# Optimization experiments

Measured on AMD Instinct MI355X. Metric: run time of the kernel, lower is better.

## Reference

```python
import jax, jax.numpy as jnp
import numpy as np

DIM = 512
HEADS = 8
HD = DIM // HEADS          # head_dim = 64
GROUPS = 32                # GroupNorm groups
EPS = 1e-5
SCALE = HD ** -0.25        # double-scale: applied to both q and k
B, H, W, L, CTX = 8, 32, 32, 77, 768


def setup_inputs() -> dict:
    key = jax.random.key(0)
    ks = jax.random.split(key, 6)
    return {
        "x": jax.random.normal(ks[0], (B, DIM, H, W), jnp.float32),
        "context": jax.random.normal(ks[1], (B, L, CTX), jnp.float32),
        "gn_gamma": jnp.ones((DIM,), jnp.float32),
        "gn_beta": jnp.zeros((DIM,), jnp.float32),
        "qkv_w": jax.random.normal(ks[2], (3 * DIM, DIM), jnp.float32) * 0.02,
        "qkv_b": jnp.zeros((3 * DIM,), jnp.float32),
        "ckv_w": jax.random.normal(ks[3], (2 * DIM, CTX), jnp.float32) * 0.02,
        "ckv_b": jnp.zeros((2 * DIM,), jnp.float32),
        "proj_w": jax.random.normal(ks[4], (DIM, DIM), jnp.float32) * 0.02,
        "proj_b": jnp.zeros((DIM,), jnp.float32),
    }


def _group_norm(x, gamma, beta):
    b, c, h, w = x.shape
    xr = x.reshape(b, GROUPS, c // GROUPS, h, w)
    mu = xr.mean(axis=(2, 3, 4), keepdims=True)
    var = xr.var(axis=(2, 3, 4), keepdims=True)
    xr = (xr - mu) * jax.lax.rsqrt(var + EPS)
    return xr.reshape(b, c, h, w) * gamma[None, :, None, None] + beta[None, :, None, None]


def reference(x, context, gn_gamma, gn_beta, qkv_w, qkv_b, ckv_w, ckv_b, proj_w, proj_b):
    b, c, h, w = x.shape
    n, d = HEADS, HD
    identity = x

    xn = _group_norm(x, gn_gamma, gn_beta)
    # 1x1 conv == channel GEMM. qkv: [b, 3*dim, h*w] -> [b, 3, n, d, hw]
    qkv = jnp.einsum('bchw,oc->bohw', xn, qkv_w) + qkv_b[None, :, None, None]
    qkv = qkv.reshape(b, 3, n, d, h * w)
    q, k, v = qkv[:, 0], qkv[:, 1], qkv[:, 2]   # each [b, n, d, hw]

    # context kv: Linear(context_dim, 2*dim) -> [b, L, 2, n, d] -> [b, n, d, L]
    ckv = jnp.einsum('blc,oc->blo', context, ckv_w) + ckv_b
    ckv = ckv.reshape(b, -1, 2, n, d)
    ck = jnp.transpose(ckv[:, :, 0], (0, 2, 3, 1))  # [b, n, d, L]
    cv = jnp.transpose(ckv[:, :, 1], (0, 2, 3, 1))
    k = jnp.concatenate([ck, k], axis=-1)           # [b, n, d, L+hw]
    v = jnp.concatenate([cv, v], axis=-1)

    # attn = (q^T * s) @ (k * s); softmax over keys
    attn = jnp.einsum('bndq,bndk->bnqk', q * SCALE, k * SCALE)
    attn = jax.nn.softmax(attn, axis=-1)
    out = jnp.einsum('bndk,bnqk->bndq', v, attn).reshape(b, c, h, w)

    out = jnp.einsum('bchw,oc->bohw', out, proj_w) + proj_b[None, :, None, None]
    return out + identity
```

## Files before the change

kernel.cpp:

```cpp
#include <hip/hip_runtime.h>

#define B_ 8
#define DIM_ 512
#define HEADS_ 8
#define HD_ 64
#define HW_ 1024
#define L_ 77
#define LP_ 80
#define CTX_ 768
#define KV_ 1101
#define KVP_ 1152
#define NPAD_ 51
#define CTX0_ 1024
#define SC_QK 0.42466089f

typedef __attribute__((ext_vector_type(8))) short bf16x8;
typedef __attribute__((ext_vector_type(4))) float f32x4;
typedef __attribute__((ext_vector_type(4))) unsigned short u16x4;

__device__ __forceinline__ unsigned short f2bf(float f) {
  union { float f; unsigned int u; } c; c.f = f;
  unsigned int u = c.u;
  return (unsigned short)((u + 0x7fffu + ((u >> 16) & 1u)) >> 16);
}
__device__ __forceinline__ float bf2f(unsigned short h) {
  union { unsigned int u; float f; } c; c.u = ((unsigned int)h) << 16;
  return c.f;
}

#define GLD_LDS16(gsrc, ldst) \
  __builtin_amdgcn_global_load_lds((const __attribute__((address_space(1))) void*)(gsrc), \
                                   (__attribute__((address_space(3))) void*)(ldst), 16, 0, 0)

__global__ __launch_bounds__(256) void prep_k(const float* __restrict__ qkv_w,
                                              const float* __restrict__ ckv_w,
                                              const float* __restrict__ proj_w,
                                              const float* __restrict__ ctx,
                                              unsigned short* __restrict__ dq,
                                              unsigned short* __restrict__ dc,
                                              unsigned short* __restrict__ dp,
                                              unsigned short* __restrict__ ctx_bf,
                                              unsigned short* __restrict__ k_s,
                                              unsigned short* __restrict__ vT) {
  int bid = blockIdx.x;
  int tid = threadIdx.x;
  if (bid < 1792) {
    int i = bid * 256 + tid;
    const float* src;
    unsigned short* dst;
    int off;
    if (i < 196608) { src = qkv_w; dst = dq; off = i; }
    else if (i < 393216) { src = ckv_w; dst = dc; off = i - 196608; }
    else { src = proj_w; dst = dp; off = i - 393216; }
    float4 v = *(const float4*)(src + (size_t)off * 4);
    u16x4 o;
    o[0] = f2bf(v.x); o[1] = f2bf(v.y); o[2] = f2bf(v.z); o[3] = f2bf(v.w);
    *(u16x4*)(dst + (size_t)off * 4) = o;
  } else if (bid < 2272) {
    int i = (bid - 1792) * 256 + tid;
    int idx = i * 4;
    int b = idx / (LP_ * CTX_);
    int rem = idx - b * (LP_ * CTX_);
    int l = rem / CTX_;
    int c = rem - l * CTX_;
    float4 v = make_float4(0.f, 0.f, 0.f, 0.f);
    if (l < L_) v = *(const float4*)&ctx[((size_t)b * L_ + l) * CTX_ + c];
    u16x4 o;
    o[0] = f2bf(v.x); o[1] = f2bf(v.y); o[2] = f2bf(v.z); o[3] = f2bf(v.w);
    *(u16x4*)(ctx_bf + idx) = o;
  } else {
    int i = (bid - 2272) * 256 + tid;
    int bh = i / (NPAD_ * 64);
    int rem = i - bh * (NPAD_ * 64);
    int row = KV_ + rem / 64;
    int d = rem & 63;
    k_s[((size_t)bh * KVP_ + row) * HD_ + d] = 0;
    vT[((size_t)bh * HD_ + d) * KVP_ + row] = 0;
  }
}

__global__ __launch_bounds__(256) void gnorm_k(const float* __restrict__ x,
                                               const float* __restrict__ gamma,
                                               const float* __restrict__ beta,
                                               unsigned short* __restrict__ xn_t) {
  __shared__ unsigned short xs[16][1032];
  __shared__ float red[8];
  const int tid = threadIdx.x;
  const int b = blockIdx.x >> 5, g = blockIdx.x & 31;
  const float* xp = x + ((size_t)b * DIM_ + g * 16) * HW_;
  float sum = 0.f, ssq = 0.f;
#pragma unroll
  for (int i = 0; i < 16; ++i) {
    float4 v = *(const float4*)&xp[i * HW_ + tid * 4];
    sum += v.x + v.y + v.z + v.w;
    ssq += v.x * v.x + v.y * v.y + v.z * v.z + v.w * v.w;
    xs[i][tid * 4 + 0] = f2bf(v.x);
    xs[i][tid * 4 + 1] = f2bf(v.y);
    xs[i][tid * 4 + 2] = f2bf(v.z);
    xs[i][tid * 4 + 3] = f2bf(v.w);
  }
#pragma unroll
  for (int off = 32; off >= 1; off >>= 1) {
    sum += __shfl_xor(sum, off, 64);
    ssq += __shfl_xor(ssq, off, 64);
  }
  if ((tid & 63) == 0) { red[(tid >> 6) * 2] = sum; red[(tid >> 6) * 2 + 1] = ssq; }
  __syncthreads();
  sum = red[0] + red[2] + red[4] + red[6];
  ssq = red[1] + red[3] + red[5] + red[7];
  float mu = sum * (1.f / 16384.f);
  float rstd = rsqrtf(ssq * (1.f / 16384.f) - mu * mu + 1e-5f);
  float a[16], c[16];
#pragma unroll
  for (int ci = 0; ci < 16; ++ci) {
    float gm = gamma[g * 16 + ci], bt = beta[g * 16 + ci];
    a[ci] = rstd * gm;
    c[ci] = bt - mu * rstd * gm;
  }
#pragma unroll
  for (int t = 0; t < 4; ++t) {
    int hw = tid + t * 256;
    unsigned short tmp[16];
#pragma unroll
    for (int ci = 0; ci < 16; ++ci)
      tmp[ci] = f2bf(bf2f(xs[ci][hw]) * a[ci] + c[ci]);
    unsigned int w[8];
#pragma unroll
    for (int j = 0; j < 8; ++j) w[j] = (unsigned int)tmp[2 * j] | ((unsigned int)tmp[2 * j + 1] << 16);
    unsigned short* dptr = &xn_t[((size_t)b * HW_ + hw) * DIM_ + g * 16];
    *(uint4*)dptr = make_uint4(w[0], w[1], w[2], w[3]);
    *(uint4*)(dptr + 8) = make_uint4(w[4], w[5], w[6], w[7]);
  }
}

template <int MODE, int BM, int BN>
__device__ __forceinline__ void gemm_body(int bid,
                                          const unsigned short* __restrict__ A,
                                          const unsigned short* __restrict__ Bt,
                                          int M, int N, int K,
                                          const float* __restrict__ bias,
                                          unsigned short* __restrict__ out_q,
                                          unsigned short* __restrict__ out_k,
                                          unsigned short* __restrict__ out_v,
                                          const float* __restrict__ xres,
                                          float* __restrict__ outf,
                                          unsigned short* sm) {
  constexpr int MR = BM / 32;
  constexpr int NR = BN / 32;
  constexpr int SLOADS = BM / 32 + BN / 32;
  unsigned short* As0 = sm;
  unsigned short* Bs0 = sm + 2 * BM * 64;
  const int tid = threadIdx.x;
  const int wid = tid >> 6, lane = tid & 63;
  const int lr = lane & 15, lg = lane >> 4;
  const int ntn = N / BN;
  const int tm = bid / ntn, tn = bid - tm * ntn;
  const int m0 = tm * BM, n0 = tn * BN;
  const int wr = wid >> 1, wc = wid & 1;
  f32x4 acc[MR][NR] = {};
  const int nkt = K >> 6;

  auto stage = [&](int bi, int kk) {
#pragma unroll
    for (int i = 0; i < BM / 32; ++i) {
      int c = i * 256 + tid;
      int row = c >> 3, ch = (c & 7) ^ (row & 7);
      GLD_LDS16(A + (size_t)(m0 + row) * K + kk + ch * 8,
                As0 + (size_t)bi * BM * 64 + (size_t)(i * 256 + wid * 64) * 8);
    }
#pragma unroll
    for (int i = 0; i < BN / 32; ++i) {
      int c = i * 256 + tid;
      int row = c >> 3, ch = (c & 7) ^ (row & 7);
      GLD_LDS16(Bt + (size_t)(n0 + row) * K + kk + ch * 8,
                Bs0 + (size_t)bi * BN * 64 + (size_t)(i * 256 + wid * 64) * 8);
    }
  };

  __builtin_amdgcn_sched_barrier(0);
  stage(0, 0);
  __builtin_amdgcn_sched_barrier(0);
  if (nkt > 1) stage(1, 64);
  __builtin_amdgcn_sched_barrier(0);

  for (int kt = 0; kt < nkt; ++kt) {
    if (kt < nkt - 1) {
      if constexpr (SLOADS == 8)      asm volatile("s_waitcnt vmcnt(8)" ::: "memory");
      else if constexpr (SLOADS == 6) asm volatile("s_waitcnt vmcnt(6)" ::: "memory");
      else                            asm volatile("s_waitcnt vmcnt(0)" ::: "memory");
    } else {
      asm volatile("s_waitcnt vmcnt(0)" ::: "memory");
    }
    __builtin_amdgcn_sched_barrier(0);
    __builtin_amdgcn_s_barrier();
    __builtin_amdgcn_sched_barrier(0);
    const unsigned short* Ab = As0 + (kt & 1) * BM * 64;
    const unsigned short* Bb = Bs0 + (kt & 1) * BN * 64;
#pragma unroll
    for (int ks = 0; ks < 2; ++ks) {
      bf16x8 af[MR], bf[NR];
#pragma unroll
      for (int mi = 0; mi < MR; ++mi)
        af[mi] = *(const bf16x8*)&Ab[(wr * (BM / 2) + mi * 16 + lr) * 64 +
                                     (((ks * 4 + lg) ^ (lr & 7)) * 8)];
#pragma unroll
      for (int nj = 0; nj < NR; ++nj)
        bf[nj] = *(const bf16x8*)&Bb[(wc * (BN / 2) + nj * 16 + lr) * 64 +
                                     (((ks * 4 + lg) ^ (lr & 7)) * 8)];
#pragma unroll
      for (int mi = 0; mi < MR; ++mi)
#pragma unroll
        for (int nj = 0; nj < NR; ++nj)
          acc[mi][nj] = __builtin_amdgcn_mfma_f32_16x16x32_bf16(af[mi], bf[nj], acc[mi][nj], 0, 0, 0);
    }
    asm volatile("s_waitcnt lgkmcnt(0)" ::: "memory");
    __builtin_amdgcn_sched_barrier(0);
    __builtin_amdgcn_s_barrier();
    __builtin_amdgcn_sched_barrier(0);
    if (kt + 2 < nkt) stage(kt & 1, (kt + 2) << 6);
  }

  if constexpr (MODE == 0) {
    const int which = n0 >> 9;
    const int bb = m0 >> 10;
    const int qibase = m0 & 1023;
    if (which == 2) {
      uint2* Vt = (uint2*)sm;
#pragma unroll
      for (int mi = 0; mi < MR; ++mi) {
#pragma unroll
        for (int nj = 0; nj < NR; ++nj) {
          int col = wc * 64 + nj * 16 + lr;
          float b = bias[n0 + col];
          unsigned int w0, w1;
          float v0 = acc[mi][nj][0] + b, v1 = acc[mi][nj][1] + b;
          float v2 = acc[mi][nj][2] + b, v3 = acc[mi][nj][3] + b;
          asm("v_cvt_pk_bf16_f32 %0, %1, %2" : "=v"(w0) : "v"(v0), "v"(v1));
          asm("v_cvt_pk_bf16_f32 %0, %1, %2" : "=v"(w1) : "v"(v2), "v"(v3));
          int chunk = (wr * 16 + mi * 4 + lg) ^ (lr * 2);
          Vt[col * 32 + chunk] = make_uint2(w0, w1);
        }
      }
      __syncthreads();
#pragma unroll
      for (int it = 0; it < 8; ++it) {
        int col = wid * 32 + it * 4 + lg;
        uint4 val = *(uint4*)&Vt[col * 32 + ((lr * 2) ^ ((col & 15) * 2))];
        int colg = n0 + col;
        int head = (colg >> 6) & 7, d = colg & 63;
        *(uint4*)&out_v[(((size_t)bb * HEADS_ + head) * HD_ + d) * KVP_ + qibase + lr * 8] = val;
      }
    } else {
      unsigned short* Tq = sm;
#pragma unroll
      for (int mi = 0; mi < MR; ++mi) {
#pragma unroll
        for (int nj = 0; nj < NR; ++nj) {
          int col = wc * 64 + nj * 16 + lr;
          float b = bias[n0 + col];
          int qr = wr * 64 + mi * 16 + lg * 4;
#pragma unroll
          for (int r = 0; r < 4; ++r)
            Tq[(qr + r) * 132 + col] = f2bf((acc[mi][nj][r] + b) * SC_QK);
        }
      }
      __syncthreads();
#pragma unroll
      for (int it = 0; it < 8; ++it) {
        int qi = wid * 32 + it * 4 + lg;
        uint2 lo = *(uint2*)&Tq[qi * 132 + lr * 8];
        uint2 hi = *(uint2*)&Tq[qi * 132 + lr * 8 + 4];
        uint4 val = make_uint4(lo.x, lo.y, hi.x, hi.y);
        int colg = n0 + lr * 8;
        int head = (colg >> 6) & 7, d = colg & 63;
        size_t bh = (size_t)bb * HEADS_ + head;
        if (which == 0)
          *(uint4*)&out_q[(bh * HW_ + qibase + qi) * HD_ + d] = val;
        else
          *(uint4*)&out_k[(bh * KVP_ + qibase + qi) * HD_ + d] = val;
      }
    }
  } else {
#pragma unroll
    for (int mi = 0; mi < MR; ++mi) {
#pragma unroll
      for (int nj = 0; nj < NR; ++nj) {
#pragma unroll
        for (int r = 0; r < 4; ++r) {
          int row = m0 + wr * (BM / 2) + mi * 16 + lg * 4 + r;
          int col = n0 + wc * (BN / 2) + nj * 16 + lr;
          float v = acc[mi][nj][r];
          if (MODE == 1) {
            int bb = row / LP_, l = row - bb * LP_;
            if (l < L_) {
              v += bias[col];
              int which = col >> 9, head = (col >> 6) & 7, d = col & 63;
              size_t bh = (size_t)bb * HEADS_ + head;
              if (which == 0) out_k[(bh * KVP_ + CTX0_ + l) * HD_ + d] = f2bf(v * SC_QK);
              else            out_v[(bh * HD_ + d) * KVP_ + CTX0_ + l] = f2bf(v);
            }
          } else {
            size_t idx = (size_t)(col >> 10) * (DIM_ * HW_) + (size_t)row * HW_ + (col & 1023);
            outf[idx] = v + bias[row] + xres[idx];
          }
        }
      }
    }
  }
}

__global__ __launch_bounds__(256, 2) void gemm_qkv_ckv_k(
    const unsigned short* __restrict__ xn_t, const unsigned short* __restrict__ qkvw,
    const unsigned short* __restrict__ ctx_bf, const unsigned short* __restrict__ ckvw,
    const float* __restrict__ qkv_b, const float* __restrict__ ckv_b,
    unsigned short* __restrict__ q_s, unsigned short* __restrict__ k_s,
    unsigned short* __restrict__ vT) {
  __shared__ unsigned short sm[2 * 256 * 64];
  int bid = blockIdx.x;
  if (bid < 80) {
    gemm_body<1, 64, 128>(bid, ctx_bf, ckvw, 640, 1024, 768, ckv_b,
                          nullptr, k_s, vT, nullptr, nullptr, sm);
  } else {
    int b = bid - 80;
    int b2 = (b & 7) * 96 + (b >> 3);
    gemm_body<0, 128, 128>(b2, xn_t, qkvw, 8192, 1536, 512, qkv_b,
                           q_s, k_s, vT, nullptr, nullptr, sm);
  }
}

__global__ __launch_bounds__(256, 2) void gemm_proj_k(
    const unsigned short* __restrict__ projw, const unsigned short* __restrict__ at_s,
    const float* __restrict__ proj_b, const float* __restrict__ x,
    float* __restrict__ out) {
  __shared__ unsigned short sm[2 * 192 * 64];
  gemm_body<2, 64, 128>(blockIdx.x, projw, at_s, 512, 8192, 512, proj_b,
                        nullptr, nullptr, nullptr, x, out, sm);
}

#define PSTRIDE 72

__device__ __forceinline__ void attn_tile64(const unsigned short* __restrict__ Ksb,
                                            const unsigned short* __restrict__ Vsb,
                                            const bf16x8 (&qf)[2][2], const bf16x8 ones,
                                            unsigned short* __restrict__ Pw0,
                                            unsigned short* __restrict__ Pw1,
                                            int lr, int lg,
                                            const int (&ro)[4], const int (&koff)[2],
                                            f32x4 (&lacc)[2], f32x4 (&acc)[2][4]) {
  f32x4 st[2][4] = {};
  __builtin_amdgcn_s_setprio(1);
#pragma unroll
  for (int ks = 0; ks < 2; ++ks) {
    bf16x8 kf[4];
#pragma unroll
    for (int t = 0; t < 4; ++t)
      kf[t] = *(const bf16x8*)&Ksb[ro[t] + koff[ks]];
#pragma unroll
    for (int t = 0; t < 4; ++t) {
      st[0][t] = __builtin_amdgcn_mfma_f32_16x16x32_bf16(kf[t], qf[0][ks], st[0][t], 0, 0, 0);
      st[1][t] = __builtin_amdgcn_mfma_f32_16x16x32_bf16(kf[t], qf[1][ks], st[1][t], 0, 0, 0);
    }
  }
  __builtin_amdgcn_s_setprio(0);
#pragma unroll
  for (int c = 0; c < 2; ++c) {
#pragma unroll
    for (int t = 0; t < 4; ++t)
#pragma unroll
      for (int r = 0; r < 4; ++r) st[c][t][r] = __builtin_amdgcn_exp2f(st[c][t][r]);
    unsigned short* Pw = c ? Pw1 : Pw0;
#pragma unroll
    for (int t = 0; t < 4; ++t) {
      unsigned int w0, w1;
      asm("v_cvt_pk_bf16_f32 %0, %1, %2" : "=v"(w0) : "v"(st[c][t][0]), "v"(st[c][t][1]));
      asm("v_cvt_pk_bf16_f32 %0, %1, %2" : "=v"(w1) : "v"(st[c][t][2]), "v"(st[c][t][3]));
      *(uint2*)&Pw[lr * PSTRIDE + t * 16 + lg * 4] = make_uint2(w0, w1);
    }
  }
#pragma unroll
  for (int ks = 0; ks < 2; ++ks) {
    bf16x8 pb0 = *(const bf16x8*)&Pw0[lr * PSTRIDE + ks * 32 + lg * 8];
    bf16x8 pb1 = *(const bf16x8*)&Pw1[lr * PSTRIDE + ks * 32 + lg * 8];
    __builtin_amdgcn_s_setprio(1);
    lacc[0] = __builtin_amdgcn_mfma_f32_16x16x32_bf16(ones, pb0, lacc[0], 0, 0, 0);
    lacc[1] = __builtin_amdgcn_mfma_f32_16x16x32_bf16(ones, pb1, lacc[1], 0, 0, 0);
#pragma unroll
    for (int dt = 0; dt < 4; ++dt) {
      bf16x8 vf = *(const bf16x8*)&Vsb[ro[dt] + koff[ks]];
      acc[0][dt] = __builtin_amdgcn_mfma_f32_16x16x32_bf16(vf, pb0, acc[0][dt], 0, 0, 0);
      acc[1][dt] = __builtin_amdgcn_mfma_f32_16x16x32_bf16(vf, pb1, acc[1][dt], 0, 0, 0);
    }
    __builtin_amdgcn_s_setprio(0);
  }
}

__global__ __launch_bounds__(256, 3) void attn_k(const unsigned short* __restrict__ q_s,
                                                 const unsigned short* __restrict__ k_s,
                                                 const unsigned short* __restrict__ vT,
                                                 unsigned short* __restrict__ at_s) {
  __shared__ unsigned short Ks[2][4096];
  __shared__ unsigned short Vs[2][4096];
  __shared__ unsigned short Pb[4][2][16 * PSTRIDE];
  const int tid = threadIdx.x;
  const int wid = tid >> 6, lane = tid & 63;
  const int lr = lane & 15, lg = lane >> 4;
  const int bidx = blockIdx.x;
  const int xcd = bidx & 7, idx = bidx >> 3;
  const int bh = xcd + 8 * (idx >> 3);
  const int qt = idx & 7;
  const int q0 = qt * 128 + wid * 32;
  const unsigned short* qp = q_s + (size_t)bh * HW_ * HD_;
  const unsigned short* kp = k_s + (size_t)bh * KVP_ * HD_;
  const unsigned short* vp = vT + (size_t)bh * HD_ * KVP_;
  unsigned short* Pw0 = Pb[wid][0];
  unsigned short* Pw1 = Pb[wid][1];

  const int srow = lane >> 3;
  const int schunk = (lane & 7) ^ srow;

  auto stage = [&](int bufi, int kk) {
#pragma unroll
    for (int jj = 0; jj < 2; ++jj) {
      GLD_LDS16(kp + (size_t)(kk + wid * 16 + jj * 8 + srow) * HD_ + schunk * 8,
                &Ks[bufi][(wid * 2 + jj) * 512]);
      GLD_LDS16(vp + (size_t)(wid * 16 + jj * 8 + srow) * KVP_ + kk + schunk * 8,
                &Vs[bufi][(wid * 2 + jj) * 512]);
    }
  };

  int ro[4], koff[2];
#pragma unroll
  for (int t = 0; t < 4; ++t) ro[t] = (t * 16 + lr) * 64;
#pragma unroll
  for (int ks = 0; ks < 2; ++ks) koff[ks] = ((ks * 4 + lg) ^ (lr & 7)) * 8;

  bf16x8 qf[2][2];
#pragma unroll
  for (int c = 0; c < 2; ++c)
#pragma unroll
    for (int ks = 0; ks < 2; ++ks)
      qf[c][ks] = *(const bf16x8*)&qp[(size_t)(q0 + c * 16 + lr) * HD_ + ks * 32 + lg * 8];

  bf16x8 ones;
#pragma unroll
  for (int j = 0; j < 8; ++j) ones[j] = (short)0x3F80;

  f32x4 acc[2][4] = {};
  f32x4 lacc[2] = {};

  __builtin_amdgcn_sched_barrier(0);
  stage(0, 0);
  __builtin_amdgcn_sched_barrier(0);
  stage(1, 64);
  __builtin_amdgcn_sched_barrier(0);

  int cur = 0;
  for (int it = 0; it < 17; ++it) {
    asm volatile("s_waitcnt vmcnt(4)" ::: "memory");
    __builtin_amdgcn_sched_barrier(0);
    __builtin_amdgcn_s_barrier();
    __builtin_amdgcn_sched_barrier(0);
    attn_tile64(Ks[cur], Vs[cur], qf, ones, Pw0, Pw1, lr, lg, ro, koff, lacc, acc);
    asm volatile("s_waitcnt lgkmcnt(0)" ::: "memory");
    __builtin_amdgcn_sched_barrier(0);
    __builtin_amdgcn_s_barrier();
    __builtin_amdgcn_sched_barrier(0);
    if (it < 16) stage(cur, (it + 2) * 64);
    cur ^= 1;
  }
  asm volatile("s_waitcnt vmcnt(0)" ::: "memory");
  __builtin_amdgcn_sched_barrier(0);
  __builtin_amdgcn_s_barrier();
  __builtin_amdgcn_sched_barrier(0);
  attn_tile64(Ks[cur], Vs[cur], qf, ones, Pw0, Pw1, lr, lg, ro, koff, lacc, acc);

  const int bb = bh >> 3, head = bh & 7;
#pragma unroll
  for (int c = 0; c < 2; ++c) {
    const float inv = 1.f / (lacc[c][0] - (float)NPAD_);
    const int qi = q0 + c * 16 + lr;
#pragma unroll
    for (int dt = 0; dt < 4; ++dt) {
      u16x4 o;
#pragma unroll
      for (int r = 0; r < 4; ++r) o[r] = f2bf(acc[c][dt][r] * inv);
      *(u16x4*)&at_s[((size_t)bb * HW_ + qi) * DIM_ + head * HD_ + dt * 16 + lg * 4] = o;
    }
  }
}

extern "C" void kernel_launch(void* const* d_in, const int* in_sizes, int n_in,
                              void* d_out, int out_size, void* d_ws, size_t ws_size,
                              hipStream_t stream) {
  (void)in_sizes; (void)n_in; (void)out_size; (void)ws_size;
  const float* x      = (const float*)d_in[0];
  const float* ctx    = (const float*)d_in[1];
  const float* gng    = (const float*)d_in[2];
  const float* gnb    = (const float*)d_in[3];
  const float* qkv_w  = (const float*)d_in[4];
  const float* qkv_b  = (const float*)d_in[5];
  const float* ckv_w  = (const float*)d_in[6];
  const float* ckv_b  = (const float*)d_in[7];
  const float* proj_w = (const float*)d_in[8];
  const float* proj_b = (const float*)d_in[9];
  float* out = (float*)d_out;

  char* ws = (char*)d_ws;
  size_t off = 0;
  auto alloc = [&](size_t bytes) {
    char* p = ws + off;
    off = (off + bytes + 255) & ~(size_t)255;
    return p;
  };
  unsigned short* xn_t    = (unsigned short*)alloc((size_t)B_ * HW_ * DIM_ * 2);
  unsigned short* ctx_bf  = (unsigned short*)alloc((size_t)B_ * LP_ * CTX_ * 2);
  unsigned short* qkvw_bf = (unsigned short*)alloc((size_t)3 * DIM_ * DIM_ * 2);
  unsigned short* ckvw_bf = (unsigned short*)alloc((size_t)2 * DIM_ * CTX_ * 2);
  unsigned short* projw_bf= (unsigned short*)alloc((size_t)DIM_ * DIM_ * 2);
  unsigned short* q_s     = (unsigned short*)alloc((size_t)64 * HW_ * HD_ * 2);
  unsigned short* k_s     = (unsigned short*)alloc((size_t)64 * KVP_ * HD_ * 2);
  unsigned short* vT      = (unsigned short*)alloc((size_t)64 * HD_ * KVP_ * 2);
  unsigned short* at_s    = (unsigned short*)alloc((size_t)B_ * HW_ * DIM_ * 2);

  prep_k<<<3088, 256, 0, stream>>>(qkv_w, ckv_w, proj_w, ctx,
                                   qkvw_bf, ckvw_bf, projw_bf, ctx_bf, k_s, vT);
  gnorm_k<<<256, 256, 0, stream>>>(x, gng, gnb, xn_t);
  gemm_qkv_ckv_k<<<848, 256, 0, stream>>>(xn_t, qkvw_bf, ctx_bf, ckvw_bf,
                                          qkv_b, ckv_b, q_s, k_s, vT);
  attn_k<<<512, 256, 0, stream>>>(q_s, k_s, vT, at_s);
  gemm_proj_k<<<512, 256, 0, stream>>>(projw_bf, at_s, proj_b, x, out);
}
```

Measured before the change: 74.82 us.

## Fuse groupnorm into prep kernel and triple-buffer GEMM with BK=32

The groupnorm work moves into the prep kernel as an extra 256 blocks, which removes one kernel launch. The GEMM body switches from a double-buffered BK=64 pipeline to a triple-buffered BK=32 pipeline with a new XOR swizzle. Each iteration now needs only one barrier, with the next stage issued right after the wait. Launch bounds rise to allow more resident blocks, trading more k-iterations and barriers for better latency hiding. The fused prep kernel now carries 33KB of LDS on every block, including the blocks that only convert weights.

```diff
diff --git a/kernel.cpp b/kernel.cpp
--- a/kernel.cpp
+++ b/kernel.cpp
@@ -32,20 +32,72 @@
   __builtin_amdgcn_global_load_lds((const __attribute__((address_space(1))) void*)(gsrc), \
                                    (__attribute__((address_space(3))) void*)(ldst), 16, 0, 0)
 
-__global__ __launch_bounds__(256) void prep_k(const float* __restrict__ qkv_w,
+__global__ __launch_bounds__(256) void prep_k(const float* __restrict__ x,
+                                              const float* __restrict__ gamma,
+                                              const float* __restrict__ beta,
+                                              const float* __restrict__ qkv_w,
                                               const float* __restrict__ ckv_w,
                                               const float* __restrict__ proj_w,
                                               const float* __restrict__ ctx,
+                                              unsigned short* __restrict__ xn_t,
                                               unsigned short* __restrict__ dq,
                                               unsigned short* __restrict__ dc,
                                               unsigned short* __restrict__ dp,
                                               unsigned short* __restrict__ ctx_bf,
                                               unsigned short* __restrict__ k_s,
                                               unsigned short* __restrict__ vT) {
+  __shared__ unsigned short xs[16][1032];
+  __shared__ float red[8];
   int bid = blockIdx.x;
   int tid = threadIdx.x;
-  if (bid < 1792) {
-    int i = bid * 256 + tid;
+  if (bid < 256) {
+    const int b = bid >> 5, g = bid & 31;
+    const float* xp = x + ((size_t)b * DIM_ + g * 16) * HW_;
+    float sum = 0.f, ssq = 0.f;
+#pragma unroll
+    for (int i = 0; i < 16; ++i) {
+      float4 v = *(const float4*)&xp[i * HW_ + tid * 4];
+      sum += v.x + v.y + v.z + v.w;
+      ssq += v.x * v.x + v.y * v.y + v.z * v.z + v.w * v.w;
+      xs[i][tid * 4 + 0] = f2bf(v.x);
+      xs[i][tid * 4 + 1] = f2bf(v.y);
+      xs[i][tid * 4 + 2] = f2bf(v.z);
+      xs[i][tid * 4 + 3] = f2bf(v.w);
+    }
+#pragma unroll
+    for (int off = 32; off >= 1; off >>= 1) {
+      sum += __shfl_xor(sum, off, 64);
+      ssq += __shfl_xor(ssq, off, 64);
+    }
+    if ((tid & 63) == 0) { red[(tid >> 6) * 2] = sum; red[(tid >> 6) * 2 + 1] = ssq; }
+    __syncthreads();
+    sum = red[0] + red[2] + red[4] + red[6];
+    ssq = red[1] + red[3] + red[5] + red[7];
+    float mu = sum * (1.f / 16384.f);
+    float rstd = rsqrtf(ssq * (1.f / 16384.f) - mu * mu + 1e-5f);
+    float a[16], c[16];
+#pragma unroll
+    for (int ci = 0; ci < 16; ++ci) {
+      float gm = gamma[g * 16 + ci], bt = beta[g * 16 + ci];
+      a[ci] = rstd * gm;
+      c[ci] = bt - mu * rstd * gm;
+    }
+#pragma unroll
+    for (int t = 0; t < 4; ++t) {
+      int hw = tid + t * 256;
+      unsigned short tmp[16];
+#pragma unroll
+      for (int ci = 0; ci < 16; ++ci)
+        tmp[ci] = f2bf(bf2f(xs[ci][hw]) * a[ci] + c[ci]);
+      unsigned int w[8];
+#pragma unroll
+      for (int j = 0; j < 8; ++j) w[j] = (unsigned int)tmp[2 * j] | ((unsigned int)tmp[2 * j + 1] << 16);
+      unsigned short* dptr = &xn_t[((size_t)b * HW_ + hw) * DIM_ + g * 16];
+      *(uint4*)dptr = make_uint4(w[0], w[1], w[2], w[3]);
+      *(uint4*)(dptr + 8) = make_uint4(w[4], w[5], w[6], w[7]);
+    }
+  } else if (bid < 2048) {
+    int i = (bid - 256) * 256 + tid;
     const float* src;
     unsigned short* dst;
     int off;
@@ -56,8 +108,8 @@
     u16x4 o;
     o[0] = f2bf(v.x); o[1] = f2bf(v.y); o[2] = f2bf(v.z); o[3] = f2bf(v.w);
     *(u16x4*)(dst + (size_t)off * 4) = o;
-  } else if (bid < 2272) {
-    int i = (bid - 1792) * 256 + tid;
+  } else if (bid < 2528) {
+    int i = (bid - 2048) * 256 + tid;
     int idx = i * 4;
     int b = idx / (LP_ * CTX_);
     int rem = idx - b * (LP_ * CTX_);
@@ -69,67 +121,13 @@
     o[0] = f2bf(v.x); o[1] = f2bf(v.y); o[2] = f2bf(v.z); o[3] = f2bf(v.w);
     *(u16x4*)(ctx_bf + idx) = o;
   } else {
-    int i = (bid - 2272) * 256 + tid;
+    int i = (bid - 2528) * 256 + tid;
     int bh = i / (NPAD_ * 64);
     int rem = i - bh * (NPAD_ * 64);
     int row = KV_ + rem / 64;
     int d = rem & 63;
     k_s[((size_t)bh * KVP_ + row) * HD_ + d] = 0;
     vT[((size_t)bh * HD_ + d) * KVP_ + row] = 0;
-  }
-}
-
-__global__ __launch_bounds__(256) void gnorm_k(const float* __restrict__ x,
-                                               const float* __restrict__ gamma,
-                                               const float* __restrict__ beta,
-                                               unsigned short* __restrict__ xn_t) {
-  __shared__ unsigned short xs[16][1032];
-  __shared__ float red[8];
-  const int tid = threadIdx.x;
-  const int b = blockIdx.x >> 5, g = blockIdx.x & 31;
-  const float* xp = x + ((size_t)b * DIM_ + g * 16) * HW_;
-  float sum = 0.f, ssq = 0.f;
-#pragma unroll
-  for (int i = 0; i < 16; ++i) {
-    float4 v = *(const float4*)&xp[i * HW_ + tid * 4];
-    sum += v.x + v.y + v.z + v.w;
-    ssq += v.x * v.x + v.y * v.y + v.z * v.z + v.w * v.w;
-    xs[i][tid * 4 + 0] = f2bf(v.x);
-    xs[i][tid * 4 + 1] = f2bf(v.y);
-    xs[i][tid * 4 + 2] = f2bf(v.z);
-    xs[i][tid * 4 + 3] = f2bf(v.w);
-  }
-#pragma unroll
-  for (int off = 32; off >= 1; off >>= 1) {
-    sum += __shfl_xor(sum, off, 64);
-    ssq += __shfl_xor(ssq, off, 64);
-  }
-  if ((tid & 63) == 0) { red[(tid >> 6) * 2] = sum; red[(tid >> 6) * 2 + 1] = ssq; }
-  __syncthreads();
-  sum = red[0] + red[2] + red[4] + red[6];
-  ssq = red[1] + red[3] + red[5] + red[7];
-  float mu = sum * (1.f / 16384.f);
-  float rstd = rsqrtf(ssq * (1.f / 16384.f) - mu * mu + 1e-5f);
-  float a[16], c[16];
-#pragma unroll
-  for (int ci = 0; ci < 16; ++ci) {
-    float gm = gamma[g * 16 + ci], bt = beta[g * 16 + ci];
-    a[ci] = rstd * gm;
-    c[ci] = bt - mu * rstd * gm;
-  }
-#pragma unroll
-  for (int t = 0; t < 4; ++t) {
-    int hw = tid + t * 256;
-    unsigned short tmp[16];
-#pragma unroll
-    for (int ci = 0; ci < 16; ++ci)
-      tmp[ci] = f2bf(bf2f(xs[ci][hw]) * a[ci] + c[ci]);
-    unsigned int w[8];
-#pragma unroll
-    for (int j = 0; j < 8; ++j) w[j] = (unsigned int)tmp[2 * j] | ((unsigned int)tmp[2 * j + 1] << 16);
-    unsigned short* dptr = &xn_t[((size_t)b * HW_ + hw) * DIM_ + g * 16];
-    *(uint4*)dptr = make_uint4(w[0], w[1], w[2], w[3]);
-    *(uint4*)(dptr + 8) = make_uint4(w[4], w[5], w[6], w[7]);
   }
 }
 
@@ -147,9 +145,11 @@
                                           unsigned short* sm) {
   constexpr int MR = BM / 32;
   constexpr int NR = BN / 32;
-  constexpr int SLOADS = BM / 32 + BN / 32;
+  constexpr int AG = BM / 64;
+  constexpr int BG = BN / 64;
+  constexpr int SLOADS = AG + BG;
   unsigned short* As0 = sm;
-  unsigned short* Bs0 = sm + 2 * BM * 64;
+  unsigned short* Bs0 = sm + 3 * BM * 32;
   const int tid = threadIdx.x;
   const int wid = tid >> 6, lane = tid & 63;
   const int lr = lane & 15, lg = lane >> 4;
@@ -158,69 +158,66 @@
   const int m0 = tm * BM, n0 = tn * BN;
   const int wr = wid >> 1, wc = wid & 1;
   f32x4 acc[MR][NR] = {};
-  const int nkt = K >> 6;
+  const int nkt = K >> 5;
 
   auto stage = [&](int bi, int kk) {
 #pragma unroll
-    for (int i = 0; i < BM / 32; ++i) {
+    for (int i = 0; i < AG; ++i) {
       int c = i * 256 + tid;
-      int row = c >> 3, ch = (c & 7) ^ (row & 7);
-      GLD_LDS16(A + (size_t)(m0 + row) * K + kk + ch * 8,
-                As0 + (size_t)bi * BM * 64 + (size_t)(i * 256 + wid * 64) * 8);
-    }
-#pragma unroll
-    for (int i = 0; i < BN / 32; ++i) {
+      int row = c >> 2, l = (c & 3) ^ ((row >> 1) & 3);
+      GLD_LDS16(A + (size_t)(m0 + row) * K + kk + l * 8,
+                As0 + (size_t)bi * BM * 32 + (size_t)c * 8);
+    }
+#pragma unroll
+    for (int i = 0; i < BG; ++i) {
       int c = i * 256 + tid;
-      int row = c >> 3, ch = (c & 7) ^ (row & 7);
-      GLD_LDS16(Bt + (size_t)(n0 + row) * K + kk + ch * 8,
-                Bs0 + (size_t)bi * BN * 64 + (size_t)(i * 256 + wid * 64) * 8);
+      int row = c >> 2, l = (c & 3) ^ ((row >> 1) & 3);
+      GLD_LDS16(Bt + (size_t)(n0 + row) * K + kk + l * 8,
+                Bs0 + (size_t)bi * BN * 32 + (size_t)c * 8);
     }
   };
 
   __builtin_amdgcn_sched_barrier(0);
   stage(0, 0);
   __builtin_amdgcn_sched_barrier(0);
-  if (nkt > 1) stage(1, 64);
-  __builtin_amdgcn_sched_barrier(0);
-
+  stage(1, 32);
+  __builtin_amdgcn_sched_barrier(0);
+
+  int cur = 0;
   for (int kt = 0; kt < nkt; ++kt) {
     if (kt < nkt - 1) {
-      if constexpr (SLOADS == 8)      asm volatile("s_waitcnt vmcnt(8)" ::: "memory");
-      else if constexpr (SLOADS == 6) asm volatile("s_waitcnt vmcnt(6)" ::: "memory");
-      else                            asm volatile("s_waitcnt vmcnt(0)" ::: "memory");
+      if constexpr (SLOADS == 4) asm volatile("s_waitcnt vmcnt(4)" ::: "memory");
+      else                       asm volatile("s_waitcnt vmcnt(3)" ::: "memory");
     } else {
       asm volatile("s_waitcnt vmcnt(0)" ::: "memory");
     }
     __builtin_amdgcn_sched_barrier(0);
     __builtin_amdgcn_s_barrier();
     __builtin_amdgcn_sched_barrier(0);
-    const unsigned short* Ab = As0 + (kt & 1) * BM * 64;
-    const unsigned short* Bb = Bs0 + (kt & 1) * BN * 64;
-#pragma unroll
-    for (int ks = 0; ks < 2; ++ks) {
-      bf16x8 af[MR], bf[NR];
-#pragma unroll
-      for (int mi = 0; mi < MR; ++mi)
-        af[mi] = *(const bf16x8*)&Ab[(wr * (BM / 2) + mi * 16 + lr) * 64 +
-                                     (((ks * 4 + lg) ^ (lr & 7)) * 8)];
+    if (kt + 2 < nkt) stage(cur == 0 ? 2 : cur - 1, (kt + 2) << 5);
+    const unsigned short* Ab = As0 + cur * BM * 32;
+    const unsigned short* Bb = Bs0 + cur * BN * 32;
+    bf16x8 af[MR], bf[NR];
+#pragma unroll
+    for (int mi = 0; mi < MR; ++mi) {
+      int row = wr * (BM / 2) + mi * 16 + lr;
+      af[mi] = *(const bf16x8*)&Ab[row * 32 + ((lg ^ ((row >> 1) & 3)) * 8)];
+    }
+#pragma unroll
+    for (int nj = 0; nj < NR; ++nj) {
+      int row = wc * (BN / 2) + nj * 16 + lr;
+      bf[nj] = *(const bf16x8*)&Bb[row * 32 + ((lg ^ ((row >> 1) & 3)) * 8)];
+    }
+#pragma unroll
+    for (int mi = 0; mi < MR; ++mi)
 #pragma unroll
       for (int nj = 0; nj < NR; ++nj)
-        bf[nj] = *(const bf16x8*)&Bb[(wc * (BN / 2) + nj * 16 + lr) * 64 +
-                                     (((ks * 4 + lg) ^ (lr & 7)) * 8)];
-#pragma unroll
-      for (int mi = 0; mi < MR; ++mi)
-#pragma unroll
-        for (int nj = 0; nj < NR; ++nj)
-          acc[mi][nj] = __builtin_amdgcn_mfma_f32_16x16x32_bf16(af[mi], bf[nj], acc[mi][nj], 0, 0, 0);
-    }
-    asm volatile("s_waitcnt lgkmcnt(0)" ::: "memory");
-    __builtin_amdgcn_sched_barrier(0);
-    __builtin_amdgcn_s_barrier();
-    __builtin_amdgcn_sched_barrier(0);
-    if (kt + 2 < nkt) stage(kt & 1, (kt + 2) << 6);
+        acc[mi][nj] = __builtin_amdgcn_mfma_f32_16x16x32_bf16(af[mi], bf[nj], acc[mi][nj], 0, 0, 0);
+    cur = (cur == 2) ? 0 : cur + 1;
   }
 
   if constexpr (MODE == 0) {
+    __syncthreads();
     const int which = n0 >> 9;
     const int bb = m0 >> 10;
     const int qibase = m0 & 1023;
@@ -309,13 +306,13 @@
   }
 }
 
-__global__ __launch_bounds__(256, 2) void gemm_qkv_ckv_k(
+__global__ __launch_bounds__(256, 3) void gemm_qkv_ckv_k(
     const unsigned short* __restrict__ xn_t, const unsigned short* __restrict__ qkvw,
     const unsigned short* __restrict__ ctx_bf, const unsigned short* __restrict__ ckvw,
     const float* __restrict__ qkv_b, const float* __restrict__ ckv_b,
     unsigned short* __restrict__ q_s, unsigned short* __restrict__ k_s,
     unsigned short* __restrict__ vT) {
-  __shared__ unsigned short sm[2 * 256 * 64];
+  __shared__ unsigned short sm[3 * 256 * 32];
   int bid = blockIdx.x;
   if (bid < 80) {
     gemm_body<1, 64, 128>(bid, ctx_bf, ckvw, 640, 1024, 768, ckv_b,
@@ -328,11 +325,11 @@
   }
 }
 
-__global__ __launch_bounds__(256, 2) void gemm_proj_k(
+__global__ __launch_bounds__(256, 4) void gemm_proj_k(
     const unsigned short* __restrict__ projw, const unsigned short* __restrict__ at_s,
     const float* __restrict__ proj_b, const float* __restrict__ x,
     float* __restrict__ out) {
-  __shared__ unsigned short sm[2 * 192 * 64];
+  __shared__ unsigned short sm[3 * 192 * 32];
   gemm_body<2, 64, 128>(blockIdx.x, projw, at_s, 512, 8192, 512, proj_b,
                         nullptr, nullptr, nullptr, x, out, sm);
 }
@@ -522,9 +519,8 @@
   unsigned short* vT      = (unsigned short*)alloc((size_t)64 * HD_ * KVP_ * 2);
   unsigned short* at_s    = (unsigned short*)alloc((size_t)B_ * HW_ * DIM_ * 2);
 
-  prep_k<<<3088, 256, 0, stream>>>(qkv_w, ckv_w, proj_w, ctx,
-                                   qkvw_bf, ckvw_bf, projw_bf, ctx_bf, k_s, vT);
-  gnorm_k<<<256, 256, 0, stream>>>(x, gng, gnb, xn_t);
+  prep_k<<<3344, 256, 0, stream>>>(x, gng, gnb, qkv_w, ckv_w, proj_w, ctx,
+                                   xn_t, qkvw_bf, ckvw_bf, projw_bf, ctx_bf, k_s, vT);
   gemm_qkv_ckv_k<<<848, 256, 0, stream>>>(xn_t, qkvw_bf, ctx_bf, ckvw_bf,
                                           qkv_b, ckv_b, q_s, k_s, vT);
   attn_k<<<512, 256, 0, stream>>>(q_s, k_s, vT, at_s);
```

Measured after the change: 75.52 us. No clear change (+0.9%).
